# Performance work log

Hardware: AMD Instinct MI355X
Metric: run time of the kernel (lower is better)

Reference implementation:

```python
import jax, jax.numpy as jnp
import numpy as np

NEG_BIG = -1.0e9  # matches tf's -1000000000.0 masking constant


def setup_inputs() -> dict:
    key = jax.random.key(0)
    k0, k1, k2 = jax.random.split(key, 3)
    B, T, F, U = 32, 2048, 512, 128
    x = jax.random.normal(k0, (B, T, F), dtype=jnp.float32)
    W1 = jax.random.normal(k1, (F, U), dtype=jnp.float32) * 0.05
    b1 = jnp.zeros((U,), dtype=jnp.float32)
    W2 = jax.random.normal(k2, (U, 1), dtype=jnp.float32) * 0.05
    b2 = jnp.zeros((1,), dtype=jnp.float32)
    return {"x": x, "W1": W1, "b1": b1, "W2": W2, "b2": b2, "k": 64}


def reference(x, W1, b1, W2, b2, k):
    # x: [B, T, F]
    # padding mask: frame is valid if any feature is nonzero
    mask = jnp.any(x != 0, axis=-1, keepdims=True).astype(x.dtype)  # [B, T, 1]
    # policy MLP scoring
    h = jax.nn.relu(jnp.einsum('btf,fu->btu', x, W1) + b1)          # [B, T, U]
    scores = jnp.einsum('btu,uo->bto', h, W2) + b2                  # [B, T, 1]
    scores = scores * mask + NEG_BIG * (1.0 - mask)
    # top-k frame selection (inference path, training=None)
    _, top_idx = jax.lax.top_k(jnp.squeeze(scores, axis=-1), k)     # [B, k]
    B, T = x.shape[0], x.shape[1]
    sel = jnp.zeros((B, T), dtype=x.dtype)
    # tf.scatter_nd adds; top-k indices are unique per row so add == set
    sel = sel.at[jnp.arange(B)[:, None], top_idx].add(1.0)          # [B, T]
    return x * sel[:, :, None]
```

## Files before the change

### kernel.cpp

```cpp
#include <hip/hip_runtime.h>
#include <stddef.h>

constexpr int B = 32;
constexpr int T = 2048;
constexpr int F = 512;
constexpr int U = 128;
constexpr float NEG_BIG = -1.0e9f;

typedef __attribute__((ext_vector_type(8))) short short8;
typedef __attribute__((ext_vector_type(4))) float f32x4;

__device__ __forceinline__ unsigned short f2bf(float f) {
    unsigned int u = __float_as_uint(f);
    u += 0x7FFFu + ((u >> 16) & 1u);
    return (unsigned short)(u >> 16);
}
__device__ __forceinline__ float bf2f(unsigned short h) {
    return __uint_as_float(((unsigned int)h) << 16);
}

__global__ __launch_bounds__(256) void prep_w(
    const float* __restrict__ W1,
    unsigned short* __restrict__ WThi,
    unsigned short* __restrict__ WTlo)
{
    const int idx = blockIdx.x * 256 + threadIdx.x;
    const int k = idx >> 7;
    const int u = idx & 127;
    const float w = W1[idx];
    const unsigned short hi = f2bf(w);
    const unsigned short lo = f2bf(w - bf2f(hi));
    WThi[(size_t)u * F + k] = hi;
    WTlo[(size_t)u * F + k] = lo;
}

constexpr int QK  = 64;
constexpr int LDK = 68;

__global__ __launch_bounds__(256) void score_kernel(
    const float* __restrict__ x,
    const unsigned short* __restrict__ WThi,
    const unsigned short* __restrict__ WTlo,
    const float* __restrict__ b1,
    const float* __restrict__ W2,
    const float* __restrict__ b2,
    float* __restrict__ scores)
{
    __shared__ __align__(16) unsigned short wh[U * LDK];
    __shared__ __align__(16) unsigned short wl[U * LDK];

    const int tid  = threadIdx.x;
    const int wid  = tid >> 6;
    const int lane = tid & 63;
    const int l15  = lane & 15;
    const int g    = lane >> 4;
    const int m0   = blockIdx.x * 64 + wid * 16;

    const float* xrow = x + (size_t)(m0 + l15) * F + g * 8;

    const int sr = tid >> 1;
    const int sc = (tid & 1) * 4;
    const unsigned short* WHrow = WThi + (size_t)sr * F;
    const unsigned short* WLrow = WTlo + (size_t)sr * F;

    f32x4 acc[8] = {};
    bool nzflag = false;

    float4 xc[4];
    xc[0] = *reinterpret_cast<const float4*>(xrow + 0);
    xc[1] = *reinterpret_cast<const float4*>(xrow + 4);
    xc[2] = *reinterpret_cast<const float4*>(xrow + 32);
    xc[3] = *reinterpret_cast<const float4*>(xrow + 36);

    for (int q = 0; q < F / QK; ++q) {
        const int kbase = q * QK;

#pragma unroll
        for (int c = 0; c < 4; ++c) {
            const int off = (sc + c) * 8;
            *reinterpret_cast<short8*>(&wh[sr * LDK + off]) =
                *reinterpret_cast<const short8*>(&WHrow[kbase + off]);
            *reinterpret_cast<short8*>(&wl[sr * LDK + off]) =
                *reinterpret_cast<const short8*>(&WLrow[kbase + off]);
        }
        __syncthreads();

        float4 xn[4];
        if (q < F / QK - 1) {
            const int nb = kbase + QK;
            xn[0] = *reinterpret_cast<const float4*>(xrow + nb);
            xn[1] = *reinterpret_cast<const float4*>(xrow + nb + 4);
            xn[2] = *reinterpret_cast<const float4*>(xrow + nb + 32);
            xn[3] = *reinterpret_cast<const float4*>(xrow + nb + 36);
        }

#pragma unroll
        for (int s = 0; s < 2; ++s) {
            const float4 a0 = xc[s * 2];
            const float4 a1 = xc[s * 2 + 1];
            const float av[8] = { a0.x, a0.y, a0.z, a0.w, a1.x, a1.y, a1.z, a1.w };
            short8 ah, al;
#pragma unroll
            for (int j = 0; j < 8; ++j) {
                const unsigned short hi = f2bf(av[j]);
                ah[j] = (short)hi;
                al[j] = (short)f2bf(av[j] - bf2f(hi));
                nzflag |= (av[j] != 0.0f);
            }
            const int kloc = s * 32 + g * 8;
#pragma unroll
            for (int nf = 0; nf < 8; ++nf) {
                const int ub = (nf * 16 + l15) * LDK + kloc;
                const short8 bh = *reinterpret_cast<const short8*>(&wh[ub]);
                const short8 bl = *reinterpret_cast<const short8*>(&wl[ub]);
                acc[nf] = __builtin_amdgcn_mfma_f32_16x16x32_bf16(ah, bh, acc[nf], 0, 0, 0);
                acc[nf] = __builtin_amdgcn_mfma_f32_16x16x32_bf16(ah, bl, acc[nf], 0, 0, 0);
                acc[nf] = __builtin_amdgcn_mfma_f32_16x16x32_bf16(al, bh, acc[nf], 0, 0, 0);
            }
        }
        __syncthreads();

        xc[0] = xn[0]; xc[1] = xn[1]; xc[2] = xn[2]; xc[3] = xn[3];
    }

    const unsigned long long nzb = __ballot(nzflag);

    float b1v[8], w2v[8];
#pragma unroll
    for (int nf = 0; nf < 8; ++nf) {
        const int u = nf * 16 + l15;
        b1v[nf] = b1[u];
        w2v[nf] = W2[u];
    }
    const float bias2 = b2[0];

#pragma unroll
    for (int r = 0; r < 4; ++r) {
        float s = 0.0f;
#pragma unroll
        for (int nf = 0; nf < 8; ++nf) {
            float h = acc[nf][r] + b1v[nf];
            h = h > 0.0f ? h : 0.0f;
            s += h * w2v[nf];
        }
        s += __shfl_xor(s, 1);
        s += __shfl_xor(s, 2);
        s += __shfl_xor(s, 4);
        s += __shfl_xor(s, 8);
        if (l15 == 0) {
            const int fr = g * 4 + r;
            const bool nz = (nzb & (0x0001000100010001ULL << fr)) != 0ULL;
            scores[m0 + fr] = nz ? (s + bias2) : NEG_BIG;
        }
    }
}

__global__ __launch_bounds__(256) void topk_kernel(
    const float* __restrict__ scores,
    const int* __restrict__ kp,
    int* __restrict__ sel)
{
    __shared__ float srow[T];

    const int b     = blockIdx.x >> 3;
    const int chunk = blockIdx.x & 7;
    const float* row = scores + (size_t)b * T;

    for (int i = threadIdx.x; i < T / 4; i += 256)
        reinterpret_cast<float4*>(srow)[i] =
            reinterpret_cast<const float4*>(row)[i];
    __syncthreads();

    const int t   = chunk * 256 + threadIdx.x;
    const float s = srow[t];
    int cnt = 0;
    for (int i = 0; i < T / 4; ++i) {
        const float4 v = reinterpret_cast<const float4*>(srow)[i];
        const int base = i * 4;
        cnt += (v.x > s) || (v.x == s && (base + 0) < t);
        cnt += (v.y > s) || (v.y == s && (base + 1) < t);
        cnt += (v.z > s) || (v.z == s && (base + 2) < t);
        cnt += (v.w > s) || (v.w == s && (base + 3) < t);
    }
    sel[(size_t)b * T + t] = (cnt < kp[0]) ? 1 : 0;
}

__global__ __launch_bounds__(256) void out_kernel(
    const float* __restrict__ x,
    const int* __restrict__ sel,
    float* __restrict__ out)
{
    __shared__ int ssel[32];

    const int fbase = blockIdx.x * 32;
    if (threadIdx.x < 32) ssel[threadIdx.x] = sel[fbase + threadIdx.x];
    __syncthreads();

    const size_t base4 = (size_t)fbase * (F / 4);
    const f32x4* x4 = reinterpret_cast<const f32x4*>(x) + base4;
    f32x4*       o4 = reinterpret_cast<f32x4*>(out) + base4;
    const f32x4 z = {0.0f, 0.0f, 0.0f, 0.0f};

#pragma unroll
    for (int it = 0; it < 16; ++it) {
        const int q  = it * 256 + threadIdx.x;
        const int fr = q >> 7;
        f32x4 v = z;
        if (ssel[fr]) v = x4[q];
        __builtin_nontemporal_store(v, &o4[q]);
    }
}

extern "C" void kernel_launch(void* const* d_in, const int* in_sizes, int n_in,
                              void* d_out, int out_size, void* d_ws, size_t ws_size,
                              hipStream_t stream)
{
    const float* x  = (const float*)d_in[0];
    const float* W1 = (const float*)d_in[1];
    const float* b1 = (const float*)d_in[2];
    const float* W2 = (const float*)d_in[3];
    const float* b2 = (const float*)d_in[4];
    const int*   kp = (const int*)d_in[5];

    char* ws = (char*)d_ws;
    unsigned short* WThi = (unsigned short*)ws;
    unsigned short* WTlo = (unsigned short*)(ws + 131072);
    float* scores        = (float*)(ws + 262144);
    int*   sel           = (int*)(ws + 524288);

    float* out = (float*)d_out;

    prep_w<<<256, 256, 0, stream>>>(W1, WThi, WTlo);
    score_kernel<<<(B * T) / 64, 256, 0, stream>>>(x, WThi, WTlo, b1, W2, b2, scores);
    topk_kernel<<<B * 8, 256, 0, stream>>>(scores, kp, sel);
    out_kernel<<<(B * T) / 32, 256, 0, stream>>>(x, sel, out);
}
```

Baseline: 129.1 us.

## Double per-wave row tile and deepen x prefetch in score kernel

Each wave now computes two 16-row M fragments instead of one, so every weight fragment read from LDS feeds twice as many MFMAs. The K-chunk staged in LDS doubles to 128, which halves the number of barriers. The x loads now use a two-slot rolling prefetch 64 elements ahead. The trade-off is more accumulator registers and more LDS per block, which may lower occupancy, and half as many blocks (512) are launched.

```diff
diff --git a/kernel.cpp b/kernel.cpp
--- a/kernel.cpp
+++ b/kernel.cpp
@@ -34,8 +34,8 @@
     WTlo[(size_t)u * F + k] = lo;
 }
 
-constexpr int QK  = 64;
-constexpr int LDK = 68;
+constexpr int QK  = 128;
+constexpr int LDK = 132;
 
 __global__ __launch_bounds__(256) void score_kernel(
     const float* __restrict__ x,
@@ -54,29 +54,36 @@
     const int lane = tid & 63;
     const int l15  = lane & 15;
     const int g    = lane >> 4;
-    const int m0   = blockIdx.x * 64 + wid * 16;
-
-    const float* xrow = x + (size_t)(m0 + l15) * F + g * 8;
+    const int wm0  = blockIdx.x * 128 + wid * 32;
+
+    const float* xr0 = x + (size_t)(wm0 + l15) * F + g * 8;
+    const float* xr1 = xr0 + (size_t)16 * F;
 
     const int sr = tid >> 1;
-    const int sc = (tid & 1) * 4;
+    const int sc = (tid & 1) * 8;
     const unsigned short* WHrow = WThi + (size_t)sr * F;
     const unsigned short* WLrow = WTlo + (size_t)sr * F;
 
-    f32x4 acc[8] = {};
-    bool nzflag = false;
-
-    float4 xc[4];
-    xc[0] = *reinterpret_cast<const float4*>(xrow + 0);
-    xc[1] = *reinterpret_cast<const float4*>(xrow + 4);
-    xc[2] = *reinterpret_cast<const float4*>(xrow + 32);
-    xc[3] = *reinterpret_cast<const float4*>(xrow + 36);
-
-    for (int q = 0; q < F / QK; ++q) {
-        const int kbase = q * QK;
-
-#pragma unroll
-        for (int c = 0; c < 4; ++c) {
+    f32x4 acc[2][8] = {};
+    bool nz0 = false, nz1 = false;
+
+    float4 p0a[2], p0b[2], p1a[2], p1b[2];
+#define ISSUE(slot, kk)                                                    \
+    do {                                                                   \
+        p0a[slot] = *reinterpret_cast<const float4*>(xr0 + (kk));          \
+        p0b[slot] = *reinterpret_cast<const float4*>(xr0 + (kk) + 4);      \
+        p1a[slot] = *reinterpret_cast<const float4*>(xr1 + (kk));          \
+        p1b[slot] = *reinterpret_cast<const float4*>(xr1 + (kk) + 4);      \
+    } while (0)
+
+    ISSUE(0, 0);
+    ISSUE(1, 32);
+
+    for (int p = 0; p < F / QK; ++p) {
+        const int kbase = p * QK;
+
+#pragma unroll
+        for (int c = 0; c < 8; ++c) {
             const int off = (sc + c) * 8;
             *reinterpret_cast<short8*>(&wh[sr * LDK + off]) =
                 *reinterpret_cast<const short8*>(&WHrow[kbase + off]);
@@ -85,27 +92,28 @@
         }
         __syncthreads();
 
-        float4 xn[4];
-        if (q < F / QK - 1) {
-            const int nb = kbase + QK;
-            xn[0] = *reinterpret_cast<const float4*>(xrow + nb);
-            xn[1] = *reinterpret_cast<const float4*>(xrow + nb + 4);
-            xn[2] = *reinterpret_cast<const float4*>(xrow + nb + 32);
-            xn[3] = *reinterpret_cast<const float4*>(xrow + nb + 36);
-        }
-
-#pragma unroll
-        for (int s = 0; s < 2; ++s) {
-            const float4 a0 = xc[s * 2];
-            const float4 a1 = xc[s * 2 + 1];
-            const float av[8] = { a0.x, a0.y, a0.z, a0.w, a1.x, a1.y, a1.z, a1.w };
-            short8 ah, al;
+#pragma unroll
+        for (int s = 0; s < 4; ++s) {
+            const int slot = s & 1;
+            const float4 a0 = p0a[slot], b0 = p0b[slot];
+            const float4 a1 = p1a[slot], b1f = p1b[slot];
+
+            const int kk = kbase + s * 32 + 64;
+            if (kk < F) ISSUE(slot, kk);
+
+            const float av0[8] = { a0.x, a0.y, a0.z, a0.w, b0.x, b0.y, b0.z, b0.w };
+            const float av1[8] = { a1.x, a1.y, a1.z, a1.w, b1f.x, b1f.y, b1f.z, b1f.w };
+            short8 ah0, al0, ah1, al1;
 #pragma unroll
             for (int j = 0; j < 8; ++j) {
-                const unsigned short hi = f2bf(av[j]);
-                ah[j] = (short)hi;
-                al[j] = (short)f2bf(av[j] - bf2f(hi));
-                nzflag |= (av[j] != 0.0f);
+                unsigned short hi = f2bf(av0[j]);
+                ah0[j] = (short)hi;
+                al0[j] = (short)f2bf(av0[j] - bf2f(hi));
+                nz0 |= (av0[j] != 0.0f);
+                hi = f2bf(av1[j]);
+                ah1[j] = (short)hi;
+                al1[j] = (short)f2bf(av1[j] - bf2f(hi));
+                nz1 |= (av1[j] != 0.0f);
             }
             const int kloc = s * 32 + g * 8;
 #pragma unroll
@@ -113,17 +121,20 @@
                 const int ub = (nf * 16 + l15) * LDK + kloc;
                 const short8 bh = *reinterpret_cast<const short8*>(&wh[ub]);
                 const short8 bl = *reinterpret_cast<const short8*>(&wl[ub]);
-                acc[nf] = __builtin_amdgcn_mfma_f32_16x16x32_bf16(ah, bh, acc[nf], 0, 0, 0);
-                acc[nf] = __builtin_amdgcn_mfma_f32_16x16x32_bf16(ah, bl, acc[nf], 0, 0, 0);
-                acc[nf] = __builtin_amdgcn_mfma_f32_16x16x32_bf16(al, bh, acc[nf], 0, 0, 0);
+                acc[0][nf] = __builtin_amdgcn_mfma_f32_16x16x32_bf16(ah0, bh, acc[0][nf], 0, 0, 0);
+                acc[0][nf] = __builtin_amdgcn_mfma_f32_16x16x32_bf16(ah0, bl, acc[0][nf], 0, 0, 0);
+                acc[0][nf] = __builtin_amdgcn_mfma_f32_16x16x32_bf16(al0, bh, acc[0][nf], 0, 0, 0);
+                acc[1][nf] = __builtin_amdgcn_mfma_f32_16x16x32_bf16(ah1, bh, acc[1][nf], 0, 0, 0);
+                acc[1][nf] = __builtin_amdgcn_mfma_f32_16x16x32_bf16(ah1, bl, acc[1][nf], 0, 0, 0);
+                acc[1][nf] = __builtin_amdgcn_mfma_f32_16x16x32_bf16(al1, bh, acc[1][nf], 0, 0, 0);
             }
         }
         __syncthreads();
-
-        xc[0] = xn[0]; xc[1] = xn[1]; xc[2] = xn[2]; xc[3] = xn[3];
-    }
-
-    const unsigned long long nzb = __ballot(nzflag);
+    }
+#undef ISSUE
+
+    const unsigned long long nzb0 = __ballot(nz0);
+    const unsigned long long nzb1 = __ballot(nz1);
 
     float b1v[8], w2v[8];
 #pragma unroll
@@ -135,22 +146,26 @@
     const float bias2 = b2[0];
 
 #pragma unroll
-    for (int r = 0; r < 4; ++r) {
-        float s = 0.0f;
-#pragma unroll
-        for (int nf = 0; nf < 8; ++nf) {
-            float h = acc[nf][r] + b1v[nf];
-            h = h > 0.0f ? h : 0.0f;
-            s += h * w2v[nf];
-        }
-        s += __shfl_xor(s, 1);
-        s += __shfl_xor(s, 2);
-        s += __shfl_xor(s, 4);
-        s += __shfl_xor(s, 8);
-        if (l15 == 0) {
-            const int fr = g * 4 + r;
-            const bool nz = (nzb & (0x0001000100010001ULL << fr)) != 0ULL;
-            scores[m0 + fr] = nz ? (s + bias2) : NEG_BIG;
+    for (int mf = 0; mf < 2; ++mf) {
+        const unsigned long long nzb = mf ? nzb1 : nzb0;
+#pragma unroll
+        for (int r = 0; r < 4; ++r) {
+            float s = 0.0f;
+#pragma unroll
+            for (int nf = 0; nf < 8; ++nf) {
+                float h = acc[mf][nf][r] + b1v[nf];
+                h = h > 0.0f ? h : 0.0f;
+                s += h * w2v[nf];
+            }
+            s += __shfl_xor(s, 1);
+            s += __shfl_xor(s, 2);
+            s += __shfl_xor(s, 4);
+            s += __shfl_xor(s, 8);
+            if (l15 == 0) {
+                const int fr = g * 4 + r;
+                const bool nz = (nzb & (0x0001000100010001ULL << fr)) != 0ULL;
+                scores[wm0 + mf * 16 + fr] = nz ? (s + bias2) : NEG_BIG;
+            }
         }
     }
 }
@@ -231,7 +246,7 @@
     float* out = (float*)d_out;
 
     prep_w<<<256, 256, 0, stream>>>(W1, WThi, WTlo);
-    score_kernel<<<(B * T) / 64, 256, 0, stream>>>(x, WThi, WTlo, b1, W2, b2, scores);
+    score_kernel<<<(B * T) / 128, 256, 0, stream>>>(x, WThi, WTlo, b1, W2, b2, scores);
     topk_kernel<<<B * 8, 256, 0, stream>>>(scores, kp, sel);
     out_kernel<<<(B * T) / 32, 256, 0, stream>>>(x, sel, out);
 }
```

After: 131.7 us. +2.1%, slower.
